# Optimization experiments

Hardware: AMD Instinct MI355X
Metric: run time of the kernel (lower is better)

Reference implementation:

```python
import jax, jax.numpy as jnp
import numpy as np

N = 256
MAX_LENGTH = 1024
BATCH = 32768


def _transition(n):
    # HiPPO-LegS transition matrices (float64 numpy, matches torch module)
    q = np.arange(n, dtype=np.float64)
    col, row = np.meshgrid(q, q)
    r = 2 * q + 1
    M = -(np.where(row >= col, r, 0) - np.diag(q))
    T = np.sqrt(np.diag(2 * q + 1))
    A = T @ M @ np.linalg.inv(T)
    B = np.diag(T)  # squeezed (N,)
    return A, B


def _build_stacked(n, max_length):
    # Bilinear (Tustin) discretization at every timescale t=1..max_length.
    A, B = _transition(n)
    ts = np.arange(1, max_length + 1, dtype=np.float64)  # (L,)
    At = A[None] / ts[:, None, None]                     # (L,N,N)
    Bt = B[None] / ts[:, None]                           # (L,N)
    I = np.eye(n)
    lhs = I[None] - At / 2                               # (L,N,N), lower triangular
    A_stacked = np.linalg.solve(lhs, I[None] + At / 2)   # (L,N,N)
    B_stacked = np.linalg.solve(lhs, Bt[..., None])[..., 0]  # (L,N)
    return A_stacked.astype(np.float32), B_stacked.astype(np.float32)


def setup_inputs() -> dict:
    key = jax.random.key(0)
    k1, k2 = jax.random.split(key)
    A_np, B_np = _build_stacked(N, MAX_LENGTH)
    return {
        "c": jax.random.normal(k1, (BATCH, N), dtype=jnp.float32),
        "f": jax.random.normal(k2, (BATCH, 1), dtype=jnp.float32),
        "A_stacked": jnp.asarray(A_np),  # (L, N, N) buffer
        "B_stacked": jnp.asarray(B_np),  # (L, N) buffer
        "t": 512,
    }


def reference(c, f, A_stacked, B_stacked, t):
    # F.linear(c, A) == c @ A.T ; then scaled add of new value f
    A = A_stacked[t]            # (N, N)
    b = B_stacked[t]            # (N,)
    return c @ A.T + b * f      # (BATCH, N)
```

## Files before the change

### kernel.cpp

```cpp
#include <hip/hip_runtime.h>
#include <cstdint>
#include <cstddef>

typedef _Float16 half8 __attribute__((ext_vector_type(8)));
typedef float f32x4 __attribute__((ext_vector_type(4)));

static constexpr int kN  = 256;
static constexpr int kKS = 8;
static constexpr int kNT = 16;
static constexpr int kWaves = 8;
static constexpr int kBM = kWaves * 16;
static constexpr size_t kLDS = (size_t)kN * kN * 2;

__global__ __launch_bounds__(512, 2) void hippo_fused(
    const float* __restrict__ c, const float* __restrict__ f,
    const float* __restrict__ A_stacked, const float* __restrict__ Bst,
    const int* __restrict__ tptr, float* __restrict__ out)
{
    extern __shared__ char lds_raw[];
    _Float16* __restrict__ As = (_Float16*)lds_raw;

    const int tid  = threadIdx.x;
    const int l    = tid & 63;
    const int wid  = tid >> 6;
    const int lo16 = l & 15;
    const int hi4  = l >> 4;
    const int t    = tptr[0];

    const float* __restrict__ asrc =
        A_stacked + (size_t)t * kN * kN + (size_t)lo16 * kN + wid * 32 + (hi4 << 3);
    f32x4 a0[kNT], a1[kNT];
    #pragma unroll
    for (int u = 0; u < kNT; ++u) {
        const float* p = asrc + (size_t)u * 16 * kN;
        a0[u] = *(const f32x4*)p;
        a1[u] = *(const f32x4*)(p + 4);
    }

    const int m0 = blockIdx.x * kBM + wid * 16;
    const float* __restrict__ cptr = c + (size_t)(m0 + lo16) * kN + (hi4 << 3);
    f32x4 cv0[kKS], cv1[kKS];
    #pragma unroll
    for (int ks = 0; ks < kKS; ++ks) {
        cv0[ks] = *(const f32x4*)(cptr + ks * 32);
        cv1[ks] = *(const f32x4*)(cptr + ks * 32 + 4);
    }

    #pragma unroll
    for (int u = 0; u < kNT; ++u) {
        half8 h;
        h[0] = (_Float16)a0[u][0]; h[1] = (_Float16)a0[u][1];
        h[2] = (_Float16)a0[u][2]; h[3] = (_Float16)a0[u][3];
        h[4] = (_Float16)a1[u][0]; h[5] = (_Float16)a1[u][1];
        h[6] = (_Float16)a1[u][2]; h[7] = (_Float16)a1[u][3];
        ((half8*)As)[u * 512 + tid] = h;
    }

    half8 af[kKS];
    #pragma unroll
    for (int ks = 0; ks < kKS; ++ks) {
        af[ks][0] = (_Float16)cv0[ks][0]; af[ks][1] = (_Float16)cv0[ks][1];
        af[ks][2] = (_Float16)cv0[ks][2]; af[ks][3] = (_Float16)cv0[ks][3];
        af[ks][4] = (_Float16)cv1[ks][0]; af[ks][5] = (_Float16)cv1[ks][1];
        af[ks][6] = (_Float16)cv1[ks][2]; af[ks][7] = (_Float16)cv1[ks][3];
    }

    const float* __restrict__ brow = Bst + (size_t)t * kN;
    float bvs[kNT];
    #pragma unroll
    for (int nt = 0; nt < kNT; ++nt) bvs[nt] = brow[nt * 16 + lo16];
    float fv[4];
    #pragma unroll
    for (int r = 0; r < 4; ++r) fv[r] = f[m0 + (hi4 << 2) + r];

    __syncthreads();

    const half8* __restrict__ Bs = (const half8*)As;
    float* __restrict__ obase = out + (size_t)(m0 + (hi4 << 2)) * kN + lo16;

    #pragma unroll
    for (int nt = 0; nt < kNT; ++nt) {
        f32x4 acc = (f32x4){0.f, 0.f, 0.f, 0.f};
        #pragma unroll
        for (int ks = 0; ks < kKS; ++ks) {
            half8 bf = Bs[(nt * kKS + ks) * 64 + l];
            acc = __builtin_amdgcn_mfma_f32_16x16x32_f16(af[ks], bf, acc, 0, 0, 0);
        }
        #pragma unroll
        for (int r = 0; r < 4; ++r)
            obase[(size_t)r * kN + nt * 16] = acc[r] + bvs[nt] * fv[r];
    }
}

extern "C" void kernel_launch(void* const* d_in, const int* in_sizes, int n_in,
                              void* d_out, int out_size, void* d_ws, size_t ws_size,
                              hipStream_t stream) {
    const float* c   = (const float*)d_in[0];
    const float* f   = (const float*)d_in[1];
    const float* A   = (const float*)d_in[2];
    const float* B   = (const float*)d_in[3];
    const int*   t   = (const int*)d_in[4];
    float* out = (float*)d_out;

    const int batch = in_sizes[0] / kN;

    hipFuncSetAttribute((const void*)hippo_fused,
                        hipFuncAttributeMaxDynamicSharedMemorySize,
                        (int)kLDS);

    hipLaunchKernelGGL(hippo_fused, dim3(batch / kBM), dim3(512), kLDS, stream,
                       c, f, A, B, t, out);
}
```

Baseline: 24.44 us.

## Split output columns across two blocks to double grid and raise occupancy

Each block now computes a 128-column half of the output, so the grid doubles and LDS per block halves, allowing more resident blocks per CU. The K loop is reordered to keep 8 accumulators and convert c fragments on the fly. The cost is that each c row tile is read by two blocks, increasing global or cache traffic. The block-index decode hardcodes 256 row tiles.

```diff
diff --git a/kernel.cpp b/kernel.cpp
--- a/kernel.cpp
+++ b/kernel.cpp
@@ -5,14 +5,14 @@
 typedef _Float16 half8 __attribute__((ext_vector_type(8)));
 typedef float f32x4 __attribute__((ext_vector_type(4)));
 
-static constexpr int kN  = 256;
-static constexpr int kKS = 8;
-static constexpr int kNT = 16;
-static constexpr int kWaves = 8;
-static constexpr int kBM = kWaves * 16;
-static constexpr size_t kLDS = (size_t)kN * kN * 2;
+static constexpr int kN   = 256;
+static constexpr int kKS  = 8;
+static constexpr int kNTb = 8;
+static constexpr int kBM  = 128;
+static constexpr int kBN  = 128;
+static constexpr size_t kLDS = (size_t)kBN * kN * 2;
 
-__global__ __launch_bounds__(512, 2) void hippo_fused(
+__global__ __launch_bounds__(512, 4) void hippo_fused(
     const float* __restrict__ c, const float* __restrict__ f,
     const float* __restrict__ A_stacked, const float* __restrict__ Bst,
     const int* __restrict__ tptr, float* __restrict__ out)
@@ -27,17 +27,22 @@
     const int hi4  = l >> 4;
     const int t    = tptr[0];
 
+    const int bid = blockIdx.x;
+    const int mb  = bid & 255;
+    const int nh  = bid >> 8;
+    const int m0  = mb * kBM + wid * 16;
+    const int n0  = nh * kBN;
+
     const float* __restrict__ asrc =
-        A_stacked + (size_t)t * kN * kN + (size_t)lo16 * kN + wid * 32 + (hi4 << 3);
-    f32x4 a0[kNT], a1[kNT];
+        A_stacked + (size_t)t * kN * kN + (size_t)(n0 + lo16) * kN + wid * 32 + (hi4 << 3);
+    f32x4 a0[kNTb], a1[kNTb];
     #pragma unroll
-    for (int u = 0; u < kNT; ++u) {
+    for (int u = 0; u < kNTb; ++u) {
         const float* p = asrc + (size_t)u * 16 * kN;
         a0[u] = *(const f32x4*)p;
         a1[u] = *(const f32x4*)(p + 4);
     }
 
-    const int m0 = blockIdx.x * kBM + wid * 16;
     const float* __restrict__ cptr = c + (size_t)(m0 + lo16) * kN + (hi4 << 3);
     f32x4 cv0[kKS], cv1[kKS];
     #pragma unroll
@@ -46,8 +51,16 @@
         cv1[ks] = *(const f32x4*)(cptr + ks * 32 + 4);
     }
 
+    const float* __restrict__ brow = Bst + (size_t)t * kN + n0;
+    float bvs[kNTb];
     #pragma unroll
-    for (int u = 0; u < kNT; ++u) {
+    for (int nt = 0; nt < kNTb; ++nt) bvs[nt] = brow[nt * 16 + lo16];
+    float fv[4];
+    #pragma unroll
+    for (int r = 0; r < 4; ++r) fv[r] = f[m0 + (hi4 << 2) + r];
+
+    #pragma unroll
+    for (int u = 0; u < kNTb; ++u) {
         half8 h;
         h[0] = (_Float16)a0[u][0]; h[1] = (_Float16)a0[u][1];
         h[2] = (_Float16)a0[u][2]; h[3] = (_Float16)a0[u][3];
@@ -55,40 +68,33 @@
         h[6] = (_Float16)a1[u][2]; h[7] = (_Float16)a1[u][3];
         ((half8*)As)[u * 512 + tid] = h;
     }
+    __syncthreads();
 
-    half8 af[kKS];
+    f32x4 acc[kNTb];
+    #pragma unroll
+    for (int i = 0; i < kNTb; ++i) acc[i] = (f32x4){0.f, 0.f, 0.f, 0.f};
+
+    const half8* __restrict__ Bs = (const half8*)As;
     #pragma unroll
     for (int ks = 0; ks < kKS; ++ks) {
-        af[ks][0] = (_Float16)cv0[ks][0]; af[ks][1] = (_Float16)cv0[ks][1];
-        af[ks][2] = (_Float16)cv0[ks][2]; af[ks][3] = (_Float16)cv0[ks][3];
-        af[ks][4] = (_Float16)cv1[ks][0]; af[ks][5] = (_Float16)cv1[ks][1];
-        af[ks][6] = (_Float16)cv1[ks][2]; af[ks][7] = (_Float16)cv1[ks][3];
+        half8 af;
+        af[0] = (_Float16)cv0[ks][0]; af[1] = (_Float16)cv0[ks][1];
+        af[2] = (_Float16)cv0[ks][2]; af[3] = (_Float16)cv0[ks][3];
+        af[4] = (_Float16)cv1[ks][0]; af[5] = (_Float16)cv1[ks][1];
+        af[6] = (_Float16)cv1[ks][2]; af[7] = (_Float16)cv1[ks][3];
+        #pragma unroll
+        for (int nt = 0; nt < kNTb; ++nt) {
+            half8 bf = Bs[(nt * kKS + ks) * 64 + l];
+            acc[nt] = __builtin_amdgcn_mfma_f32_16x16x32_f16(af, bf, acc[nt], 0, 0, 0);
+        }
     }
 
-    const float* __restrict__ brow = Bst + (size_t)t * kN;
-    float bvs[kNT];
+    float* __restrict__ obase = out + (size_t)(m0 + (hi4 << 2)) * kN + n0 + lo16;
     #pragma unroll
-    for (int nt = 0; nt < kNT; ++nt) bvs[nt] = brow[nt * 16 + lo16];
-    float fv[4];
-    #pragma unroll
-    for (int r = 0; r < 4; ++r) fv[r] = f[m0 + (hi4 << 2) + r];
-
-    __syncthreads();
-
-    const half8* __restrict__ Bs = (const half8*)As;
-    float* __restrict__ obase = out + (size_t)(m0 + (hi4 << 2)) * kN + lo16;
-
-    #pragma unroll
-    for (int nt = 0; nt < kNT; ++nt) {
-        f32x4 acc = (f32x4){0.f, 0.f, 0.f, 0.f};
-        #pragma unroll
-        for (int ks = 0; ks < kKS; ++ks) {
-            half8 bf = Bs[(nt * kKS + ks) * 64 + l];
-            acc = __builtin_amdgcn_mfma_f32_16x16x32_f16(af[ks], bf, acc, 0, 0, 0);
-        }
+    for (int nt = 0; nt < kNTb; ++nt) {
         #pragma unroll
         for (int r = 0; r < 4; ++r)
-            obase[(size_t)r * kN + nt * 16] = acc[r] + bvs[nt] * fv[r];
+            obase[(size_t)r * kN + nt * 16] = acc[nt][r] + bvs[nt] * fv[r];
     }
 }
 
@@ -108,6 +114,6 @@
                         hipFuncAttributeMaxDynamicSharedMemorySize,
                         (int)kLDS);
 
-    hipLaunchKernelGGL(hippo_fused, dim3(batch / kBM), dim3(512), kLDS, stream,
+    hipLaunchKernelGGL(hippo_fused, dim3((batch / kBM) * 2), dim3(512), kLDS, stream,
                        c, f, A, B, t, out);
 }
```

After: 28.20 us. +15.4%, slower.
